# Performance work log

Measured on AMD Instinct MI355X. Metric: run time of the kernel, lower is better.

The kernel has to match this reference:

```python
import jax, jax.numpy as jnp
import numpy as np

B, N, D = 16, 1369, 1024
HID, NH = 512, 8
SCALE = np.sqrt(D // NH)


def _pos_encoding_2d(n, d):
    ps = int(np.sqrt(n))  # 37; n is a perfect square here
    div = jnp.exp(jnp.arange(0, d // 2, 2, dtype=jnp.float32) * (-np.log(10000.0) / (d // 2)))
    rows = (jnp.arange(n) // ps).astype(jnp.float32)
    cols = (jnp.arange(n) % ps).astype(jnp.float32)
    def interleave(s, c):
        return jnp.stack([s, c], axis=-1).reshape(n, -1)
    half_row = interleave(jnp.sin(rows[:, None] * div), jnp.cos(rows[:, None] * div))
    half_col = interleave(jnp.sin(cols[:, None] * div), jnp.cos(cols[:, None] * div))
    return jnp.concatenate([half_row, half_col], axis=-1)  # [n, d]


def _center_bias(n, strength=0.3):
    ps = int(np.sqrt(n))
    c = ps // 2
    y, x = jnp.meshgrid(jnp.arange(ps, dtype=jnp.float32), jnp.arange(ps, dtype=jnp.float32), indexing='ij')
    d2 = (x - c) ** 2 + (y - c) ** 2
    sigma = ps / 6.0
    return (jnp.exp(-d2 / (2.0 * sigma ** 2)).reshape(-1)) * strength  # [n]


def setup_inputs() -> dict:
    key = jax.random.key(0)
    ks = jax.random.split(key, 16)
    s = 0.02
    return {
        'patch_tokens': jax.random.normal(ks[0], (B, N, D), dtype=jnp.float32),
        'curiosity_score': jax.random.uniform(ks[1], (B,), dtype=jnp.float32),
        'Wq': jax.random.normal(ks[2], (D, D), dtype=jnp.float32) * s,
        'bq': jax.random.uniform(ks[3], (D,), minval=-0.05, maxval=0.05, dtype=jnp.float32),
        'Wk': jax.random.normal(ks[4], (D, D), dtype=jnp.float32) * s,
        'bk': jax.random.uniform(ks[5], (D,), minval=-0.05, maxval=0.05, dtype=jnp.float32),
        'Wv': jax.random.normal(ks[6], (D, D), dtype=jnp.float32) * s,
        'bv': jnp.zeros((D,), dtype=jnp.float32),
        'Wc1': jax.random.normal(ks[7], (1, HID // 8), dtype=jnp.float32) * s,
        'bc1': jnp.zeros((HID // 8,), dtype=jnp.float32),
        'Wc2': jax.random.normal(ks[8], (HID // 8, NH), dtype=jnp.float32) * s,
        'bc2': jnp.zeros((NH,), dtype=jnp.float32),
        'Wp1': jax.random.normal(ks[9], (D, HID), dtype=jnp.float32) * s,
        'bp1': jnp.zeros((HID,), dtype=jnp.float32),
        'Wp2': jax.random.normal(ks[10], (HID, HID // 4), dtype=jnp.float32) * s,
        'bp2': jnp.zeros((HID // 4,), dtype=jnp.float32),
        'adaptive_weight': jnp.float32(0.5),
    }


def reference(patch_tokens, curiosity_score, Wq, bq, Wk, bk, Wv, bv,
              Wc1, bc1, Wc2, bc2, Wp1, bp1, Wp2, bp2, adaptive_weight):
    b, n, d = patch_tokens.shape
    x = patch_tokens + _pos_encoding_2d(n, d)[None]  # [B,N,D]

    q = x @ Wq + bq
    k = x @ Wk + bk
    v = x @ Wv + bv

    scores = jnp.einsum('bqd,bkd->bqk', q, k) / SCALE          # [B,N,N]
    attn = jax.nn.softmax(scores, axis=-1)                     # dropout p=0 / eval
    attended = jnp.einsum('bqk,bkd->bqd', attn, v)             # [B,N,D]

    cb = _center_bias(n)[None]                                 # [1,N]
    VAR_EPS = 1e-6

    pa = attn.mean(axis=1) + cb
    # fallback chain (data-dependent in torch; expressed with jnp.where)
    pa2 = jnp.diagonal(attn, axis1=-2, axis2=-1) + cb
    pa = jnp.where(jnp.var(pa, ddof=1) < VAR_EPS, pa2, pa)
    pa3 = attn.max(axis=-1) + cb
    pa = jnp.where(jnp.var(pa, ddof=1) < VAR_EPS, pa3, pa)
    norms = jnp.linalg.norm(x, axis=-1)
    noise = jax.random.normal(jax.random.key(42), norms.shape, dtype=norms.dtype) * 0.1 * jnp.std(norms, ddof=1)
    pa = jnp.where(jnp.var(pa, ddof=1) < VAR_EPS, norms + noise, pa)

    pa = pa / (pa.sum(axis=-1, keepdims=True) + 1e-8)

    # curiosity modulation
    h = jax.nn.relu(curiosity_score[:, None] @ Wc1 + bc1)
    cm = jax.nn.sigmoid(h @ Wc2 + bc2)                         # [B,NH]
    cw = cm.mean(axis=-1, keepdims=True)                       # [B,1]
    modulated = pa * (1.0 + cw)
    fa = adaptive_weight * modulated + (1.0 - adaptive_weight) * pa

    fa = jnp.clip(fa, 1e-8, None)
    fa = fa / (fa.sum(axis=-1, keepdims=True) + 1e-8)

    weighted = jnp.sum(attended * fa[..., None], axis=1)       # [B,D]
    focal = jax.nn.relu(weighted @ Wp1 + bp1) @ Wp2 + bp2      # [B,HID//4]
    return focal, fa
```

## Files before the change

### kernel.cpp

```cpp
#include <hip/hip_runtime.h>
#include <hip/hip_bf16.h>
#include <cstdint>

#define B_   16
#define N_   1369
#define NP   1536
#define D_   1024
#define NQKV 3072

typedef __bf16 bf16x8_t __attribute__((ext_vector_type(8)));
typedef __bf16 bf16x4_t __attribute__((ext_vector_type(4)));
typedef float  f32x4_t  __attribute__((ext_vector_type(4)));

__device__ __forceinline__ float  bf2f(__bf16 x) { return (float)x; }
__device__ __forceinline__ __bf16 f2bf(float x)  { return (__bf16)x; }

#define GLOAD_LDS16(g, l) __builtin_amdgcn_global_load_lds( \
    (const __attribute__((address_space(1))) void*)(g),     \
    (__attribute__((address_space(3))) void*)(l), 16, 0, 0)

__global__ __launch_bounds__(256)
void pos_kernel(float* __restrict__ pos)
{
    const int idx = blockIdx.x * 256 + threadIdx.x;
    if (idx >= N_ * D_) return;
    const int n = idx >> 10, f = idx & 1023;
    const int row = n / 37, col = n - row * 37;
    const float base = (f < 512) ? (float)row : (float)col;
    const int  t2   = (f & 511) >> 1;
    const float dv  = __expf(-0.03597789207803197f * (float)t2);
    const float ang = base * dv;
    pos[idx] = (f & 1) ? cosf(ang) : sinf(ang);
}

__global__ __launch_bounds__(256)
void addpos_kernel(const float* __restrict__ patch, const float* __restrict__ pos,
                   __bf16* __restrict__ X)
{
    const long tid = (long)blockIdx.x * 256 + threadIdx.x;
    const long e   = tid * 4;
    const int  f   = (int)(e & 1023);
    const long nb  = e >> 10;
    const int  n   = (int)(nb % NP);
    const long b   = nb / NP;
    bf16x4_t o;
    if (n < N_) {
        const float4 p = *(const float4*)(patch + ((b * N_ + n) << 10) + f);
        const float4 q = *(const float4*)(pos + ((long)n << 10) + f);
        o[0] = f2bf(p.x + q.x); o[1] = f2bf(p.y + q.y);
        o[2] = f2bf(p.z + q.z); o[3] = f2bf(p.w + q.w);
    } else {
        o[0] = o[1] = o[2] = o[3] = f2bf(0.f);
    }
    *(bf16x4_t*)(X + e) = o;
}

__global__ __launch_bounds__(256)
void wcast_kernel(const float* __restrict__ W0, const float* __restrict__ W1,
                  const float* __restrict__ W2,
                  __bf16* __restrict__ T0, __bf16* __restrict__ T1, __bf16* __restrict__ T2)
{
    const float* W = blockIdx.z == 0 ? W0 : (blockIdx.z == 1 ? W1 : W2);
    __bf16*      T = blockIdx.z == 0 ? T0 : (blockIdx.z == 1 ? T1 : T2);
    __shared__ float tile[64][65];
    const int o0 = blockIdx.x * 64, i0 = blockIdx.y * 64;
    const int t = threadIdx.x;
    const int tr = t >> 4, tc = (t & 15) * 4;
    #pragma unroll
    for (int rr = 0; rr < 64; rr += 16) {
        float4 v = *(const float4*)(W + (long)(i0 + rr + tr) * 1024 + o0 + tc);
        tile[rr + tr][tc + 0] = v.x; tile[rr + tr][tc + 1] = v.y;
        tile[rr + tr][tc + 2] = v.z; tile[rr + tr][tc + 3] = v.w;
    }
    __syncthreads();
    #pragma unroll
    for (int rr = 0; rr < 64; rr += 16) {
        bf16x4_t o;
        o[0] = f2bf(tile[tc + 0][rr + tr]); o[1] = f2bf(tile[tc + 1][rr + tr]);
        o[2] = f2bf(tile[tc + 2][rr + tr]); o[3] = f2bf(tile[tc + 3][rr + tr]);
        *(bf16x4_t*)(T + (long)(o0 + rr + tr) * 1024 + i0 + tc) = o;
    }
}

__global__ __launch_bounds__(256)
void bcat_kernel(const float* __restrict__ bq, const float* __restrict__ bk,
                 const float* __restrict__ bv, float* __restrict__ bcat)
{
    const int i = blockIdx.x * 256 + threadIdx.x;
    if (i >= NQKV) return;
    const int p = i >> 10, j = i & 1023;
    bcat[i] = p == 0 ? bq[j] : (p == 1 ? bk[j] : bv[j]);
}

template<int HAS_BIAS>
__global__ __launch_bounds__(512, 2)
void gemm256(const __bf16* __restrict__ A, const __bf16* __restrict__ Bt,
             __bf16* __restrict__ C, const float* __restrict__ bias,
             int lda, int ldb, int ldc, int Kd, float scale,
             long sA, long sB, long sC, int tilesN, int tilesPerBatch, int cpx)
{
    __shared__ __bf16 lds[65536];
    const int bid = blockIdx.x;
    const int vt  = (bid & 7) * cpx + (bid >> 3);
    const int bz  = vt / tilesPerBatch;
    const int rem = vt - bz * tilesPerBatch;
    const int ty  = rem / tilesN;
    const int tx  = rem - ty * tilesN;
    A  += (long)bz * sA;  Bt += (long)bz * sB;  C += (long)bz * sC;
    const int m0 = ty * 256, n0 = tx * 256;

    const int t  = threadIdx.x;
    const int w  = t >> 6, l = t & 63;
    const int wr = w >> 2, wc = w & 3;
    const int lr = l & 15, lh = l >> 4;

    const int laneF  = (lr * 64 + ((lh * 16) ^ (((lr >> 3) & 1) << 5))) >> 1;
    const int rstage = w * 16 + (l >> 2);
    const int kstage = ((l & 3) * 8) ^ (((l >> 5) & 1) << 4);

    const __bf16* Ag = A  + (long)(m0 + rstage) * lda + kstage;
    const __bf16* Bg = Bt + (long)(n0 + rstage) * ldb + kstage;
    __bf16* dA = lds + (w * 2) * 512;
    __bf16* dB = lds + 16384 + (w * 2) * 512;

#define SA_(buf, half, kt) do {                                       \
    const __bf16* g_ = Ag + (long)(half) * 128 * lda + (kt) * 64;     \
    __bf16* d_ = dA + (buf) * 32768 + (half) * 8192;                  \
    GLOAD_LDS16(g_, d_); GLOAD_LDS16(g_ + 32, d_ + 512); } while (0)
#define SB_(buf, half, kt) do {                                       \
    const __bf16* g_ = Bg + (long)(half) * 128 * ldb + (kt) * 64;     \
    __bf16* d_ = dB + (buf) * 32768 + (half) * 8192;                  \
    GLOAD_LDS16(g_, d_); GLOAD_LDS16(g_ + 32, d_ + 512); } while (0)

    f32x4_t acc[8][4] = {};
    bf16x8_t bfr[4][2];

#define BREADS_() do { const __bf16* bp_ = lds + cbB + laneF;                              \
    bfr[0][0] = *(const bf16x8_t*)(bp_);        bfr[0][1] = *(const bf16x8_t*)(bp_ + 512); \
    bfr[1][0] = *(const bf16x8_t*)(bp_ + 1024); bfr[1][1] = *(const bf16x8_t*)(bp_ + 1536);\
    bfr[2][0] = *(const bf16x8_t*)(bp_ + 2048); bfr[2][1] = *(const bf16x8_t*)(bp_ + 2560);\
    bfr[3][0] = *(const bf16x8_t*)(bp_ + 3072); bfr[3][1] = *(const bf16x8_t*)(bp_ + 3584);} while (0)

#define PHASE_(p, P0R, STG, VMW) do {                                                  \
    const __bf16* ap_ = lds + cbase + wr * 8192 + (p) * 2048 + laneF;                  \
    bf16x8_t a00 = *(const bf16x8_t*)(ap_);                                            \
    bf16x8_t a01 = *(const bf16x8_t*)(ap_ + 512);                                      \
    bf16x8_t a10 = *(const bf16x8_t*)(ap_ + 1024);                                     \
    bf16x8_t a11 = *(const bf16x8_t*)(ap_ + 1536);                                     \
    P0R;                                                                               \
    STG;                                                                               \
    __builtin_amdgcn_s_barrier();                                                      \
    asm volatile("s_waitcnt lgkmcnt(0)" ::: "memory");                                 \
    __builtin_amdgcn_sched_barrier(0);                                                 \
    __builtin_amdgcn_s_setprio(1);                                                     \
    _Pragma("unroll") for (int nn = 0; nn < 4; ++nn)                                   \
      acc[(p)*2+0][nn] = __builtin_amdgcn_mfma_f32_16x16x32_bf16(a00, bfr[nn][0], acc[(p)*2+0][nn], 0, 0, 0); \
    _Pragma("unroll") for (int nn = 0; nn < 4; ++nn)                                   \
      acc[(p)*2+1][nn] = __builtin_amdgcn_mfma_f32_16x16x32_bf16(a10, bfr[nn][0], acc[(p)*2+1][nn], 0, 0, 0); \
    _Pragma("unroll") for (int nn = 0; nn < 4; ++nn)                                   \
      acc[(p)*2+0][nn] = __builtin_amdgcn_mfma_f32_16x16x32_bf16(a01, bfr[nn][1], acc[(p)*2+0][nn], 0, 0, 0); \
    _Pragma("unroll") for (int nn = 0; nn < 4; ++nn)                                   \
      acc[(p)*2+1][nn] = __builtin_amdgcn_mfma_f32_16x16x32_bf16(a11, bfr[nn][1], acc[(p)*2+1][nn], 0, 0, 0); \
    __builtin_amdgcn_s_setprio(0);                                                     \
    VMW;                                                                               \
    __builtin_amdgcn_s_barrier();                                                      \
  } while (0)

    const int NT = Kd >> 6;
    SA_(0, 0, 0); SA_(0, 1, 0); SB_(0, 0, 0); SB_(0, 1, 0);
    SB_(1, 0, 1); SB_(1, 1, 1);
    asm volatile("s_waitcnt vmcnt(4)" ::: "memory");
    __builtin_amdgcn_s_barrier();

    for (int tk = 0; tk < NT; ++tk) {
        const int c  = tk & 1, o = c ^ 1;
        const int t1 = (tk + 1 < NT) ? tk + 1 : NT - 1;
        const int t2 = (tk + 2 < NT) ? tk + 2 : NT - 1;
        const int cbase = c * 32768;
        const int cbB   = cbase + 16384 + wc * 4096;
        PHASE_(0, BREADS_(), SA_(o, 0, t1), ((void)0));
        PHASE_(1, ((void)0), SA_(o, 1, t1), ((void)0));
        PHASE_(2, ((void)0), SB_(c, 0, t2), ((void)0));
        PHASE_(3, ((void)0), SB_(c, 1, t2),
               asm volatile("s_waitcnt vmcnt(4)" ::: "memory"));
    }

    #pragma unroll
    for (int mi = 0; mi < 8; ++mi) {
        const int row = m0 + wr * 128 + mi * 16 + lh * 4;
        #pragma unroll
        for (int nn = 0; nn < 4; ++nn) {
            const int col = n0 + wc * 64 + nn * 16 + lr;
            const float bb = HAS_BIAS ? bias[col] : 0.0f;
            #pragma unroll
            for (int q = 0; q < 4; ++q)
                C[(long)(row + q) * ldc + col] = f2bf(acc[mi][nn][q] * scale + bb);
        }
    }
#undef SA_
#undef SB_
#undef BREADS_
#undef PHASE_
}

__global__ __launch_bounds__(256)
void softmax_kernel(__bf16* __restrict__ S)
{
    const int q = blockIdx.x, b = blockIdx.y;
    __bf16* row = S + ((long)b * NP + q) * NP;
    const int t = threadIdx.x;
    float v[6];
    float m = -1e30f;
    #pragma unroll
    for (int i = 0; i < 6; ++i) {
        const int k = t + i * 256;
        float x = -1e30f;
        if (k < N_) x = bf2f(row[k]);
        v[i] = x;
        m = fmaxf(m, x);
    }
    __shared__ float red[8];
    #pragma unroll
    for (int o = 32; o; o >>= 1) m = fmaxf(m, __shfl_xor(m, o));
    if (!(t & 63)) red[t >> 6] = m;
    __syncthreads();
    m = fmaxf(fmaxf(red[0], red[1]), fmaxf(red[2], red[3]));
    float s = 0.f;
    #pragma unroll
    for (int i = 0; i < 6; ++i) {
        const int k = t + i * 256;
        if (k < N_) { const float e = __expf(v[i] - m); v[i] = e; s += e; }
    }
    #pragma unroll
    for (int o = 32; o; o >>= 1) s += __shfl_xor(s, o);
    if (!(t & 63)) red[4 + (t >> 6)] = s;
    __syncthreads();
    s = red[4] + red[5] + red[6] + red[7];
    const float inv = 1.f / s;
    #pragma unroll
    for (int i = 0; i < 6; ++i) {
        const int k = t + i * 256;
        if (k < N_)      row[k] = f2bf(v[i] * inv);
        else             row[k] = f2bf(0.f);
    }
}

template<int WEIGHTED>
__global__ __launch_bounds__(256)
void colsum_kernel(const __bf16* __restrict__ attn, const float* __restrict__ wv,
                   float* __restrict__ out)
{
    const int k = blockIdx.x * 256 + threadIdx.x;
    const int b = blockIdx.y;
    const int q0 = blockIdx.z * 172;
    const int q1 = (q0 + 172 < N_) ? q0 + 172 : N_;
    if (k >= N_) return;
    const __bf16* base = attn + (long)b * NP * NP + k;
    float s = 0.f;
    for (int q = q0; q < q1; ++q) {
        float a = bf2f(base[(long)q * NP]);
        if (WEIGHTED) a *= wv[b * NP + q];
        s += a;
    }
    atomicAdd(out + b * NP + k, s);
}

__global__ __launch_bounds__(256)
void fa_kernel(const float* __restrict__ pa_raw, const float* __restrict__ curiosity,
               const float* __restrict__ Wc1, const float* __restrict__ bc1,
               const float* __restrict__ Wc2, const float* __restrict__ bc2,
               const float* __restrict__ aw_p,
               float* __restrict__ fa_ws, float* __restrict__ out_fa)
{
    const int b = blockIdx.x, t = threadIdx.x;
    __shared__ float hsh[64];
    __shared__ float red[8];
    __shared__ float cwsh;
    if (t < 64) hsh[t] = fmaxf(0.f, curiosity[b] * Wc1[t] + bc1[t]);
    __syncthreads();
    if (t < 8) {
        float a = bc2[t];
        for (int j = 0; j < 64; ++j) a += hsh[j] * Wc2[j * 8 + t];
        red[t] = 1.f / (1.f + __expf(-a));
    }
    __syncthreads();
    if (t == 0) {
        float cw = 0.f;
        for (int i = 0; i < 8; ++i) cw += red[i];
        cwsh = cw * 0.125f;
    }
    __syncthreads();
    const float aw   = aw_p[0];
    const float modf = 1.f + aw * cwsh;
    const float sig  = 37.f / 6.f;
    const float inv2s2 = 1.f / (2.f * sig * sig);
    float pv[6];
    float s1 = 0.f;
    #pragma unroll
    for (int i = 0; i < 6; ++i) {
        const int k = t + i * 256;
        float p = 0.f;
        if (k < N_) {
            const int y = k / 37, x = k - y * 37;
            const float d2 = (float)((x - 18) * (x - 18) + (y - 18) * (y - 18));
            const float cb = 0.3f * __expf(-d2 * inv2s2);
            p = pa_raw[b * NP + k] * (1.f / 1369.f) + cb;
        }
        pv[i] = p; s1 += p;
    }
    #pragma unroll
    for (int o = 32; o; o >>= 1) s1 += __shfl_xor(s1, o);
    __syncthreads();
    if (!(t & 63)) red[t >> 6] = s1;
    __syncthreads();
    s1 = red[0] + red[1] + red[2] + red[3];
    const float inv1 = 1.f / (s1 + 1e-8f);
    float s2 = 0.f;
    #pragma unroll
    for (int i = 0; i < 6; ++i) {
        const int k = t + i * 256;
        if (k < N_) {
            const float f = fmaxf(pv[i] * inv1 * modf, 1e-8f);
            pv[i] = f; s2 += f;
        }
    }
    #pragma unroll
    for (int o = 32; o; o >>= 1) s2 += __shfl_xor(s2, o);
    if (!(t & 63)) red[4 + (t >> 6)] = s2;
    __syncthreads();
    s2 = red[4] + red[5] + red[6] + red[7];
    const float inv2 = 1.f / (s2 + 1e-8f);
    #pragma unroll
    for (int i = 0; i < 6; ++i) {
        const int k = t + i * 256;
        if (k < N_) {
            const float f = pv[i] * inv2;
            fa_ws[b * NP + k]  = f;
            out_fa[b * N_ + k] = f;
        }
    }
}

__global__ __launch_bounds__(256)
void weighted_kernel(const float* __restrict__ g, const __bf16* __restrict__ V,
                     int ldv, float* __restrict__ wout)
{
    const int b  = blockIdx.y;
    const int k0 = blockIdx.x * 86;
    const int k1 = (k0 + 86 < N_) ? k0 + 86 : N_;
    const int d  = threadIdx.x * 4;
    float a0 = 0, a1 = 0, a2 = 0, a3 = 0;
    const __bf16* vb = V + (long)b * NP * ldv + d;
    for (int k = k0; k < k1; ++k) {
        const float gv = g[b * NP + k];
        bf16x4_t vv = *(const bf16x4_t*)(vb + (long)k * ldv);
        a0 += gv * bf2f(vv[0]); a1 += gv * bf2f(vv[1]);
        a2 += gv * bf2f(vv[2]); a3 += gv * bf2f(vv[3]);
    }
    atomicAdd(wout + b * D_ + d + 0, a0);
    atomicAdd(wout + b * D_ + d + 1, a1);
    atomicAdd(wout + b * D_ + d + 2, a2);
    atomicAdd(wout + b * D_ + d + 3, a3);
}

__global__ __launch_bounds__(256)
void focal_kernel(const float* __restrict__ weighted, const float* __restrict__ Wp1,
                  const float* __restrict__ bp1, const float* __restrict__ Wp2,
                  const float* __restrict__ bp2, float* __restrict__ out)
{
    const int b = blockIdx.x, t = threadIdx.x;
    __shared__ float wsh[1024];
    __shared__ float hsh[512];
    for (int i = t; i < 1024; i += 256) wsh[i] = weighted[b * 1024 + i];
    __syncthreads();
    for (int j = t; j < 512; j += 256) {
        float a = bp1[j];
        for (int d2 = 0; d2 < 1024; ++d2) a += wsh[d2] * Wp1[d2 * 512 + j];
        hsh[j] = fmaxf(a, 0.f);
    }
    __syncthreads();
    for (int o = t; o < 128; o += 256) {
        float a = bp2[o];
        for (int j = 0; j < 512; ++j) a += hsh[j] * Wp2[j * 128 + o];
        out[b * 128 + o] = a;
    }
}

extern "C" void kernel_launch(void* const* d_in, const int* in_sizes, int n_in,
                              void* d_out, int out_size, void* d_ws, size_t ws_size,
                              hipStream_t stream)
{
    const float* patch     = (const float*)d_in[0];
    const float* curiosity = (const float*)d_in[1];
    const float* Wq  = (const float*)d_in[2];
    const float* bq  = (const float*)d_in[3];
    const float* Wk  = (const float*)d_in[4];
    const float* bk  = (const float*)d_in[5];
    const float* Wv  = (const float*)d_in[6];
    const float* bv  = (const float*)d_in[7];
    const float* Wc1 = (const float*)d_in[8];
    const float* bc1 = (const float*)d_in[9];
    const float* Wc2 = (const float*)d_in[10];
    const float* bc2 = (const float*)d_in[11];
    const float* Wp1 = (const float*)d_in[12];
    const float* bp1 = (const float*)d_in[13];
    const float* Wp2 = (const float*)d_in[14];
    const float* bp2 = (const float*)d_in[15];
    const float* aw  = (const float*)d_in[16];
    float* out = (float*)d_out;

    char* ws = (char*)d_ws;
    size_t off = 0;
    auto alloc = [&](size_t bytes) -> char* {
        char* p = ws + off;
        off += (bytes + 255) & ~(size_t)255;
        return p;
    };
    float*  pos  = (float*) alloc((size_t)N_ * D_ * 4);
    __bf16* X    = (__bf16*)alloc((size_t)B_ * NP * D_ * 2);
    __bf16* WT   = (__bf16*)alloc((size_t)3 * D_ * D_ * 2);
    const size_t S_BYTES = (size_t)B_ * NP * NP * 2;
    if (off < S_BYTES) off = S_BYTES;
    __bf16* S    = (__bf16*)ws;
    __bf16* QKV  = (__bf16*)alloc((size_t)B_ * NP * NQKV * 2);
    float*  pa   = (float*) alloc((size_t)B_ * NP * 4);
    float*  faw  = (float*) alloc((size_t)B_ * NP * 4);
    float*  gbuf = (float*) alloc((size_t)B_ * NP * 4);
    float*  wsum = (float*) alloc((size_t)B_ * D_ * 4);
    float*  bcat = (float*) alloc((size_t)NQKV * 4);

    (void)hipMemsetAsync(pa,   0, (size_t)B_ * NP * 4, stream);
    (void)hipMemsetAsync(gbuf, 0, (size_t)B_ * NP * 4, stream);
    (void)hipMemsetAsync(wsum, 0, (size_t)B_ * D_ * 4, stream);

    pos_kernel<<<(N_ * D_ + 255) / 256, 256, 0, stream>>>(pos);
    addpos_kernel<<<(int)((size_t)B_ * NP * D_ / 4 / 256), 256, 0, stream>>>(patch, pos, X);
    {
        dim3 g(16, 16, 3);
        wcast_kernel<<<g, 256, 0, stream>>>(Wq, Wk, Wv,
                                            WT, WT + D_ * D_, WT + 2 * D_ * D_);
    }
    bcat_kernel<<<(NQKV + 255) / 256, 256, 0, stream>>>(bq, bk, bv, bcat);
    {
        const int nwg = 96 * 12;
        gemm256<1><<<nwg, 512, 0, stream>>>(X, WT, QKV, bcat,
                                            D_, D_, NQKV, D_, 1.0f,
                                            0, 0, 0, 12, nwg, nwg / 8);
    }
    {
        const int nwg = 36 * B_;
        gemm256<0><<<nwg, 512, 0, stream>>>(QKV, QKV + D_, S, nullptr,
                                            NQKV, NQKV, NP, D_,
                                            0.08838834764831845f,
                                            (long)NP * NQKV, (long)NP * NQKV,
                                            (long)NP * NP, 6, 36, nwg / 8);
    }
    {
        dim3 g(N_, B_);
        softmax_kernel<<<g, 256, 0, stream>>>(S);
    }
    {
        dim3 g(6, B_, 8);
        colsum_kernel<0><<<g, 256, 0, stream>>>(S, nullptr, pa);
    }
    fa_kernel<<<B_, 256, 0, stream>>>(pa, curiosity, Wc1, bc1, Wc2, bc2, aw,
                                      faw, out + B_ * 128);
    {
        dim3 g(6, B_, 8);
        colsum_kernel<1><<<g, 256, 0, stream>>>(S, faw, gbuf);
    }
    {
        dim3 g(16, B_);
        weighted_kernel<<<g, 256, 0, stream>>>(gbuf, QKV + 2 * D_, NQKV, wsum);
    }
    focal_kernel<<<B_, 256, 0, stream>>>(wsum, Wp1, bp1, Wp2, bp2, out);
}
```

Measured before the change: 537.0 us.

## Triple-buffer GEMM A tiles and vectorize softmax and column-sum kernels

The GEMM LDS layout becomes a three-stage ring for A and a two-stage buffer for B, prefetching two K-steps ahead with conditional staging and a drain at the tail. This should hide more global-load latency, at the cost of more LDS per block (160 KB), which may reduce occupancy. Softmax now uses 8-wide bf16 vector loads and stores per thread. The column-sum kernel is restructured so each block covers 16 query rows and all columns with 8-wide vector loads, replacing strided scalar column reads at the price of more atomics.

```diff
diff --git a/kernel.cpp b/kernel.cpp
--- a/kernel.cpp
+++ b/kernel.cpp
@@ -99,7 +99,7 @@
              int lda, int ldb, int ldc, int Kd, float scale,
              long sA, long sB, long sC, int tilesN, int tilesPerBatch, int cpx)
 {
-    __shared__ __bf16 lds[65536];
+    __shared__ __bf16 lds[81920];
     const int bid = blockIdx.x;
     const int vt  = (bid & 7) * cpx + (bid >> 3);
     const int bz  = vt / tilesPerBatch;
@@ -120,16 +120,16 @@
 
     const __bf16* Ag = A  + (long)(m0 + rstage) * lda + kstage;
     const __bf16* Bg = Bt + (long)(n0 + rstage) * ldb + kstage;
-    __bf16* dA = lds + (w * 2) * 512;
-    __bf16* dB = lds + 16384 + (w * 2) * 512;
+    __bf16* dA = lds + w * 1024;
+    __bf16* dB = lds + 49152 + w * 1024;
 
 #define SA_(buf, half, kt) do {                                       \
     const __bf16* g_ = Ag + (long)(half) * 128 * lda + (kt) * 64;     \
-    __bf16* d_ = dA + (buf) * 32768 + (half) * 8192;                  \
+    __bf16* d_ = dA + (buf) * 16384 + (half) * 8192;                  \
     GLOAD_LDS16(g_, d_); GLOAD_LDS16(g_ + 32, d_ + 512); } while (0)
 #define SB_(buf, half, kt) do {                                       \
     const __bf16* g_ = Bg + (long)(half) * 128 * ldb + (kt) * 64;     \
-    __bf16* d_ = dB + (buf) * 32768 + (half) * 8192;                  \
+    __bf16* d_ = dB + (buf) * 16384 + (half) * 8192;                  \
     GLOAD_LDS16(g_, d_); GLOAD_LDS16(g_ + 32, d_ + 512); } while (0)
 
     f32x4_t acc[8][4] = {};
@@ -168,21 +168,24 @@
 
     const int NT = Kd >> 6;
     SA_(0, 0, 0); SA_(0, 1, 0); SB_(0, 0, 0); SB_(0, 1, 0);
-    SB_(1, 0, 1); SB_(1, 1, 1);
-    asm volatile("s_waitcnt vmcnt(4)" ::: "memory");
+    SA_(1, 0, 1); SA_(1, 1, 1); SB_(1, 0, 1); SB_(1, 1, 1);
+    asm volatile("s_waitcnt vmcnt(8)" ::: "memory");
     __builtin_amdgcn_s_barrier();
 
+    int ab = 0;
     for (int tk = 0; tk < NT; ++tk) {
-        const int c  = tk & 1, o = c ^ 1;
-        const int t1 = (tk + 1 < NT) ? tk + 1 : NT - 1;
-        const int t2 = (tk + 2 < NT) ? tk + 2 : NT - 1;
-        const int cbase = c * 32768;
-        const int cbB   = cbase + 16384 + wc * 4096;
-        PHASE_(0, BREADS_(), SA_(o, 0, t1), ((void)0));
-        PHASE_(1, ((void)0), SA_(o, 1, t1), ((void)0));
-        PHASE_(2, ((void)0), SB_(c, 0, t2), ((void)0));
-        PHASE_(3, ((void)0), SB_(c, 1, t2),
-               asm volatile("s_waitcnt vmcnt(4)" ::: "memory"));
+        const int bb = tk & 1;
+        const int st = (tk + 2 < NT);
+        const int a2 = (ab + 2 >= 3) ? ab - 1 : ab + 2;
+        const int cbase = ab * 16384;
+        const int cbB   = 49152 + bb * 16384 + wc * 4096;
+        PHASE_(0, BREADS_(), if (st) SA_(a2, 0, tk + 2), ((void)0));
+        PHASE_(1, ((void)0), if (st) SA_(a2, 1, tk + 2), ((void)0));
+        PHASE_(2, ((void)0), if (st) SB_(bb, 0, tk + 2), ((void)0));
+        PHASE_(3, ((void)0), if (st) SB_(bb, 1, tk + 2),
+               if (st) { asm volatile("s_waitcnt vmcnt(8)" ::: "memory"); }
+               else    { asm volatile("s_waitcnt vmcnt(0)" ::: "memory"); });
+        ab = (ab + 1 == 3) ? 0 : ab + 1;
     }
 
     #pragma unroll
@@ -191,10 +194,10 @@
         #pragma unroll
         for (int nn = 0; nn < 4; ++nn) {
             const int col = n0 + wc * 64 + nn * 16 + lr;
-            const float bb = HAS_BIAS ? bias[col] : 0.0f;
+            const float bb2 = HAS_BIAS ? bias[col] : 0.0f;
             #pragma unroll
             for (int q = 0; q < 4; ++q)
-                C[(long)(row + q) * ldc + col] = f2bf(acc[mi][nn][q] * scale + bb);
+                C[(long)(row + q) * ldc + col] = f2bf(acc[mi][nn][q] * scale + bb2);
         }
     }
 #undef SA_
@@ -209,15 +212,16 @@
     const int q = blockIdx.x, b = blockIdx.y;
     __bf16* row = S + ((long)b * NP + q) * NP;
     const int t = threadIdx.x;
-    float v[6];
+    const int k8 = t * 8;
+    float v[8];
     float m = -1e30f;
-    #pragma unroll
-    for (int i = 0; i < 6; ++i) {
-        const int k = t + i * 256;
-        float x = -1e30f;
-        if (k < N_) x = bf2f(row[k]);
-        v[i] = x;
-        m = fmaxf(m, x);
+    if (t < 192) {
+        bf16x8_t raw = *(const bf16x8_t*)(row + k8);
+        #pragma unroll
+        for (int i = 0; i < 8; ++i) {
+            const float x = (k8 + i < N_) ? bf2f(raw[i]) : -1e30f;
+            v[i] = x; m = fmaxf(m, x);
+        }
     }
     __shared__ float red[8];
     #pragma unroll
@@ -226,10 +230,11 @@
     __syncthreads();
     m = fmaxf(fmaxf(red[0], red[1]), fmaxf(red[2], red[3]));
     float s = 0.f;
-    #pragma unroll
-    for (int i = 0; i < 6; ++i) {
-        const int k = t + i * 256;
-        if (k < N_) { const float e = __expf(v[i] - m); v[i] = e; s += e; }
+    if (t < 192) {
+        #pragma unroll
+        for (int i = 0; i < 8; ++i) {
+            if (k8 + i < N_) { const float e = __expf(v[i] - m); v[i] = e; s += e; }
+        }
     }
     #pragma unroll
     for (int o = 32; o; o >>= 1) s += __shfl_xor(s, o);
@@ -237,11 +242,12 @@
     __syncthreads();
     s = red[4] + red[5] + red[6] + red[7];
     const float inv = 1.f / s;
-    #pragma unroll
-    for (int i = 0; i < 6; ++i) {
-        const int k = t + i * 256;
-        if (k < N_)      row[k] = f2bf(v[i] * inv);
-        else             row[k] = f2bf(0.f);
+    if (t < 192) {
+        bf16x8_t o8;
+        #pragma unroll
+        for (int i = 0; i < 8; ++i)
+            o8[i] = f2bf((k8 + i < N_) ? v[i] * inv : 0.f);
+        *(bf16x8_t*)(row + k8) = o8;
     }
 }
 
@@ -250,19 +256,22 @@
 void colsum_kernel(const __bf16* __restrict__ attn, const float* __restrict__ wv,
                    float* __restrict__ out)
 {
-    const int k = blockIdx.x * 256 + threadIdx.x;
-    const int b = blockIdx.y;
-    const int q0 = blockIdx.z * 172;
-    const int q1 = (q0 + 172 < N_) ? q0 + 172 : N_;
-    if (k >= N_) return;
-    const __bf16* base = attn + (long)b * NP * NP + k;
-    float s = 0.f;
+    const int t = threadIdx.x;
+    if (t >= 192) return;
+    const int b  = blockIdx.y;
+    const int q0 = blockIdx.x * 16;
+    const int q1 = (q0 + 16 < N_) ? q0 + 16 : N_;
+    const int k8 = t * 8;
+    float s[8] = {};
+    const __bf16* base = attn + (long)b * NP * NP + k8;
     for (int q = q0; q < q1; ++q) {
-        float a = bf2f(base[(long)q * NP]);
-        if (WEIGHTED) a *= wv[b * NP + q];
-        s += a;
-    }
-    atomicAdd(out + b * NP + k, s);
+        bf16x8_t v = *(const bf16x8_t*)(base + (long)q * NP);
+        const float wq = WEIGHTED ? wv[b * NP + q] : 1.0f;
+        #pragma unroll
+        for (int i = 0; i < 8; ++i) s[i] += wq * bf2f(v[i]);
+    }
+    #pragma unroll
+    for (int i = 0; i < 8; ++i) atomicAdd(out + b * NP + k8 + i, s[i]);
 }
 
 __global__ __launch_bounds__(256)
@@ -460,13 +469,13 @@
         softmax_kernel<<<g, 256, 0, stream>>>(S);
     }
     {
-        dim3 g(6, B_, 8);
+        dim3 g(86, B_);
         colsum_kernel<0><<<g, 256, 0, stream>>>(S, nullptr, pa);
     }
     fa_kernel<<<B_, 256, 0, stream>>>(pa, curiosity, Wc1, bc1, Wc2, bc2, aw,
                                       faw, out + B_ * 128);
     {
-        dim3 g(6, B_, 8);
+        dim3 g(86, B_);
         colsum_kernel<1><<<g, 256, 0, stream>>>(S, faw, gbuf);
     }
     {
```

After: 617.9 us. +15.1%, slower.
